# Kernel tuning notes

Hardware: AMD Instinct MI355X
Metric: run time of the kernel (lower is better)

## Reference

```python
import jax, jax.numpy as jnp
import numpy as np

B, S, D, H = 2, 2048, 1024, 16
DK = D // H


def setup_inputs() -> dict:
    key = jax.random.key(0)
    ks = jax.random.split(key, 8)
    scale = 1.0 / np.sqrt(D)
    inp = {
        "query": jax.random.normal(ks[0], (B, S, D), dtype=jnp.float32),
        "key": jax.random.normal(ks[1], (B, S, D), dtype=jnp.float32),
        "value": jax.random.normal(ks[2], (B, S, D), dtype=jnp.float32),
        # causal mask, broadcastable over batch and heads
        "mask": jnp.tril(jnp.ones((S, S), dtype=jnp.int32))[None, None, :, :],
        "W_q": jax.random.normal(ks[3], (D, D), dtype=jnp.float32) * scale,
        "W_k": jax.random.normal(ks[4], (D, D), dtype=jnp.float32) * scale,
        "W_v": jax.random.normal(ks[5], (D, D), dtype=jnp.float32) * scale,
        "W_o": jax.random.normal(ks[6], (D, D), dtype=jnp.float32) * scale,
    }
    return inp


def _split_heads(t):
    Bb, Ss, _ = t.shape
    return t.reshape(Bb, Ss, H, DK).transpose(0, 2, 1, 3)  # [B,H,S,DK]


def reference(query, key, value, mask, W_q, W_k, W_v, W_o):
    # Linear(d,d,bias=False): y = x @ W^T (torch stores weight as [out,in])
    Q = _split_heads(query @ W_q.T)
    K = _split_heads(key @ W_k.T)
    V = _split_heads(value @ W_v.T)
    scores = jnp.einsum("bhqd,bhkd->bhqk", Q, K) / jnp.sqrt(jnp.float32(DK))
    scores = jnp.where(mask == 0, -jnp.inf, scores)
    weights = jax.nn.softmax(scores, axis=-1)
    weights = jnp.nan_to_num(weights, nan=0.0)  # fully-masked rows -> 0
    # dropout is identity at inference
    x = jnp.einsum("bhqk,bhkd->bhqd", weights, V)
    x = x.transpose(0, 2, 1, 3).reshape(B, S, D)
    return x @ W_o.T
```

## Files before the change

### kernel.cpp

```cpp
#include <hip/hip_runtime.h>
#include <hip/hip_bf16.h>

#define D_MODEL 1024
#define NHEAD   16
#define HDK     64
#define SEQ     2048
#define BATCH   2
#define BS      (BATCH * SEQ)

typedef __attribute__((ext_vector_type(8))) short bf16x8;
typedef __attribute__((ext_vector_type(4))) float f32x4;

__device__ __forceinline__ unsigned short f2bf(float f) {
    unsigned u = __builtin_bit_cast(unsigned, f);
    u += 0x7fffu + ((u >> 16) & 1u);
    return (unsigned short)(u >> 16);
}

__device__ __forceinline__ unsigned pack_hi(float x, float y) {
    return __builtin_amdgcn_perm(__builtin_bit_cast(unsigned, y),
                                 __builtin_bit_cast(unsigned, x), 0x07060302u);
}

typedef const void __attribute__((address_space(1))) gas_void;
typedef void __attribute__((address_space(3))) las_void;

__device__ __forceinline__ void gll16(const void* g, void* l) {
    __builtin_amdgcn_global_load_lds((gas_void*)g, (las_void*)l, 16, 0, 0);
}

__device__ __forceinline__ void cast_body(const float* __restrict__ src,
                                          unsigned short* __restrict__ dst, int i) {
    const float4* p = (const float4*)src + (size_t)i * 2;
    float4 a = p[0], b = p[1];
    ushort4 lo = make_ushort4(f2bf(a.x), f2bf(a.y), f2bf(a.z), f2bf(a.w));
    ushort4 hi = make_ushort4(f2bf(b.x), f2bf(b.y), f2bf(b.z), f2bf(b.w));
    ushort4* q = (ushort4*)dst + (size_t)i * 2;
    q[0] = lo; q[1] = hi;
}

__global__ __launch_bounds__(256)
void cast_act(const float* a, const float* b, const float* c,
              unsigned short* oa, unsigned short* ob, unsigned short* oc, int n8) {
    int i = blockIdx.x * 256 + threadIdx.x;
    if (i >= n8) return;
    const float* s = blockIdx.y == 0 ? a : blockIdx.y == 1 ? b : c;
    unsigned short* d = blockIdx.y == 0 ? oa : blockIdx.y == 1 ? ob : oc;
    cast_body(s, d, i);
}

__global__ __launch_bounds__(256)
void cast_wt(const float* a, const float* b, const float* c, const float* dd,
             unsigned short* oa, unsigned short* ob, unsigned short* oc, unsigned short* od, int n8) {
    int i = blockIdx.x * 256 + threadIdx.x;
    if (i >= n8) return;
    const float* s = blockIdx.y == 0 ? a : blockIdx.y == 1 ? b : blockIdx.y == 2 ? c : dd;
    unsigned short* d = blockIdx.y == 0 ? oa : blockIdx.y == 1 ? ob : blockIdx.y == 2 ? oc : od;
    cast_body(s, d, i);
}

__device__ __forceinline__ void gemm_kloop128(const unsigned short* __restrict__ X,
                                              const unsigned short* __restrict__ W,
                                              unsigned short* As, unsigned short* Bs,
                                              int bm, int bn, f32x4 acc[4][4]) {
    const int t    = threadIdx.x;
    const int w    = t >> 6;
    const int L    = t & 63;
    const int quad = L >> 4;
    const int lm   = L & 15;
    const int r8   = L >> 3;
    const int sl   = L & 7;
    const int xcol = ((sl ^ r8) & 7) * 8;
    const int wr   = (w >> 1) * 64;
    const int wc   = (w & 1) * 64;

    for (int kt = 0; kt < D_MODEL; kt += 64) {
        __syncthreads();
        #pragma unroll
        for (int i = 0; i < 4; ++i) {
            int c = w * 4 + i;
            gll16(X + (size_t)(bm + c * 8 + r8) * D_MODEL + kt + xcol, &As[c * 512]);
        }
        #pragma unroll
        for (int i = 0; i < 4; ++i) {
            int c = w * 4 + i;
            gll16(W + (size_t)(bn + c * 8 + r8) * D_MODEL + kt + xcol, &Bs[c * 512]);
        }
        __syncthreads();

        #pragma unroll
        for (int ch = 0; ch < 2; ++ch) {
            bf16x8 af[4], bfr[4];
            #pragma unroll
            for (int ms = 0; ms < 4; ++ms) {
                int row = wr + ms * 16 + lm;
                af[ms] = *(const bf16x8*)&As[row * 64 + (((ch * 4 + quad) ^ (row & 7)) * 8)];
            }
            #pragma unroll
            for (int ns = 0; ns < 4; ++ns) {
                int row = wc + ns * 16 + lm;
                bfr[ns] = *(const bf16x8*)&Bs[row * 64 + (((ch * 4 + quad) ^ (row & 7)) * 8)];
            }
            #pragma unroll
            for (int ms = 0; ms < 4; ++ms)
                #pragma unroll
                for (int ns = 0; ns < 4; ++ns)
                    acc[ms][ns] = __builtin_amdgcn_mfma_f32_16x16x32_bf16(
                        af[ms], bfr[ns], acc[ms][ns], 0, 0, 0);
        }
    }
}

__device__ __forceinline__ void gemm_kloop64(const unsigned short* __restrict__ X,
                                             const unsigned short* __restrict__ W,
                                             unsigned short* As, unsigned short* Bs,
                                             int bm, int bn, f32x4 acc[2][4]) {
    const int t    = threadIdx.x;
    const int w    = t >> 6;
    const int L    = t & 63;
    const int quad = L >> 4;
    const int lm   = L & 15;
    const int r8   = L >> 3;
    const int sl   = L & 7;
    const int xcol = ((sl ^ r8) & 7) * 8;

    for (int kt = 0; kt < D_MODEL; kt += 64) {
        __syncthreads();
        #pragma unroll
        for (int i = 0; i < 4; ++i) {
            int c = w * 4 + i;
            gll16(X + (size_t)(bm + c * 8 + r8) * D_MODEL + kt + xcol, &As[c * 512]);
        }
        #pragma unroll
        for (int i = 0; i < 2; ++i) {
            int c = w * 2 + i;
            gll16(W + (size_t)(bn + c * 8 + r8) * D_MODEL + kt + xcol, &Bs[c * 512]);
        }
        __syncthreads();

        #pragma unroll
        for (int ch = 0; ch < 2; ++ch) {
            bf16x8 af[2], bfr[4];
            #pragma unroll
            for (int ms = 0; ms < 2; ++ms) {
                int row = w * 32 + ms * 16 + lm;
                af[ms] = *(const bf16x8*)&As[row * 64 + (((ch * 4 + quad) ^ (row & 7)) * 8)];
            }
            #pragma unroll
            for (int ns = 0; ns < 4; ++ns) {
                int row = ns * 16 + lm;
                bfr[ns] = *(const bf16x8*)&Bs[row * 64 + (((ch * 4 + quad) ^ (row & 7)) * 8)];
            }
            #pragma unroll
            for (int ms = 0; ms < 2; ++ms)
                #pragma unroll
                for (int ns = 0; ns < 4; ++ns)
                    acc[ms][ns] = __builtin_amdgcn_mfma_f32_16x16x32_bf16(
                        af[ms], bfr[ns], acc[ms][ns], 0, 0, 0);
        }
    }
}

__global__ __launch_bounds__(256, 3)
void proj_gemm(const unsigned short* __restrict__ qx, const unsigned short* __restrict__ kx,
               const unsigned short* __restrict__ vx, const unsigned short* __restrict__ wq,
               const unsigned short* __restrict__ wk, const unsigned short* __restrict__ wv,
               unsigned short* __restrict__ Qp, unsigned short* __restrict__ Kp,
               unsigned short* __restrict__ VT) {
    __shared__ __align__(16) unsigned short As[128 * 64];
    __shared__ __align__(16) unsigned short Bs[128 * 64];

    const int p = blockIdx.z;
    const unsigned short* X = p == 0 ? qx : p == 1 ? kx : vx;
    const unsigned short* W = p == 0 ? wq : p == 1 ? wk : wv;
    const int bm = blockIdx.y * 128, bn = blockIdx.x * 128;

    f32x4 acc[4][4];
    #pragma unroll
    for (int ms = 0; ms < 4; ++ms)
        #pragma unroll
        for (int ns = 0; ns < 4; ++ns)
            acc[ms][ns] = (f32x4){0.f, 0.f, 0.f, 0.f};

    gemm_kloop128(X, W, As, Bs, bm, bn, acc);

    const int t = threadIdx.x, w = t >> 6, L = t & 63, quad = L >> 4, lm = L & 15;
    const int wr = (w >> 1) * 64, wc = (w & 1) * 64;
    if (p == 2) {
        const int b    = bm >> 11;
        const int s_in = (bm & (SEQ - 1)) + wr;
        #pragma unroll
        for (int ms = 0; ms < 4; ++ms)
            #pragma unroll
            for (int ns = 0; ns < 4; ++ns) {
                int dg = bn + wc + ns * 16 + lm;
                int h  = dg >> 6, d = dg & 63;
                ushort4 pk = make_ushort4(f2bf(acc[ms][ns][0]), f2bf(acc[ms][ns][1]),
                                          f2bf(acc[ms][ns][2]), f2bf(acc[ms][ns][3]));
                *(ushort4*)&VT[((size_t)((b * NHEAD + h) * HDK + d)) * SEQ +
                               s_in + ms * 16 + quad * 4] = pk;
            }
    } else {
        unsigned short* Y = p == 0 ? Qp : Kp;
        const float scl = p == 0 ? 0.125f : 1.0f;
        #pragma unroll
        for (int ms = 0; ms < 4; ++ms)
            #pragma unroll
            for (int ns = 0; ns < 4; ++ns)
                #pragma unroll
                for (int r = 0; r < 4; ++r)
                    Y[(size_t)(bm + wr + ms * 16 + quad * 4 + r) * D_MODEL +
                      bn + wc + ns * 16 + lm] = f2bf(acc[ms][ns][r] * scl);
    }
}

__global__ __launch_bounds__(256)
void out_gemm(const unsigned short* __restrict__ X, const unsigned short* __restrict__ W,
              float* __restrict__ Y) {
    __shared__ __align__(16) unsigned short As[128 * 64];
    __shared__ __align__(16) unsigned short Bs[64 * 64];
    const int bm = blockIdx.y * 128, bn = blockIdx.x * 64;

    f32x4 acc[2][4];
    #pragma unroll
    for (int ms = 0; ms < 2; ++ms)
        #pragma unroll
        for (int ns = 0; ns < 4; ++ns)
            acc[ms][ns] = (f32x4){0.f, 0.f, 0.f, 0.f};

    gemm_kloop64(X, W, As, Bs, bm, bn, acc);

    const int t = threadIdx.x, w = t >> 6, L = t & 63, quad = L >> 4, lm = L & 15;
    #pragma unroll
    for (int ms = 0; ms < 2; ++ms)
        #pragma unroll
        for (int ns = 0; ns < 4; ++ns)
            #pragma unroll
            for (int r = 0; r < 4; ++r)
                Y[(size_t)(bm + w * 32 + ms * 16 + quad * 4 + r) * D_MODEL +
                  bn + ns * 16 + lm] = acc[ms][ns][r];
}

__global__ __launch_bounds__(256, 3)
void attn_mfma(const unsigned short* __restrict__ Q, const unsigned short* __restrict__ K,
               const unsigned short* __restrict__ VT, unsigned short* __restrict__ A) {
    __shared__ __align__(16) unsigned short Ks[2][64 * 72];
    __shared__ __align__(16) unsigned short Vs[2][64 * 72];
    __shared__ __align__(16) unsigned short Ps[4 * 16 * 72];

    const int t    = threadIdx.x;
    const int w    = t >> 6;
    const int L    = t & 63;
    const int quad = L >> 4;
    const int lm   = L & 15;
    const int h    = blockIdx.y;
    const int b    = blockIdx.z;
    const size_t hb  = (size_t)b * SEQ * D_MODEL + h * HDK;
    const size_t vhb = (size_t)(b * NHEAD + h) * HDK;

    const int srow = t >> 2;
    const int sc   = (t & 3) * 16;
    const unsigned short* kp = K + hb + (size_t)srow * D_MODEL + sc;
    const unsigned short* vp = VT + (vhb + srow) * SEQ + sc;
    unsigned short* ps = &Ps[w * 16 * 72];

    for (int half = 0; half < 2; ++half) {
        const int qt   = half ? 31 - (int)blockIdx.x : (int)blockIdx.x;
        const int q0   = qt * 64;
        const int qrow = q0 + w * 16 + lm;

        bf16x8 Qf0, Qf1;
        {
            const unsigned short* qp = Q + hb + (size_t)qrow * D_MODEL + quad * 8;
            Qf0 = *(const bf16x8*)qp;
            Qf1 = *(const bf16x8*)(qp + 32);
        }

        f32x4 Oacc[4];
        #pragma unroll
        for (int nt = 0; nt < 4; ++nt) Oacc[nt] = (f32x4){0.f, 0.f, 0.f, 0.f};
        float m_run = -INFINITY, l_run = 0.f;

        float4 kr0 = *(const float4*)kp;
        float4 kr1 = *(const float4*)(kp + 8);
        float4 vr0 = *(const float4*)vp;
        float4 vr1 = *(const float4*)(vp + 8);
        *(float4*)&Ks[0][srow * 72 + sc]     = kr0;
        *(float4*)&Ks[0][srow * 72 + sc + 8] = kr1;
        *(float4*)&Vs[0][srow * 72 + sc]     = vr0;
        *(float4*)&Vs[0][srow * 72 + sc + 8] = vr1;
        if (qt >= 1) {
            kr0 = *(const float4*)(kp + (size_t)64 * D_MODEL);
            kr1 = *(const float4*)(kp + (size_t)64 * D_MODEL + 8);
            vr0 = *(const float4*)(vp + 64);
            vr1 = *(const float4*)(vp + 64 + 8);
        }
        __syncthreads();

        int bb = 0;
        for (int kt = 0; kt <= qt; ++kt) {
            const int k0 = kt * 64;
            const unsigned short* Kc = Ks[bb];
            const unsigned short* Vc = Vs[bb];
            if (kt < qt) {
                unsigned short* Kn = Ks[bb ^ 1];
                unsigned short* Vn = Vs[bb ^ 1];
                *(float4*)&Kn[srow * 72 + sc]     = kr0;
                *(float4*)&Kn[srow * 72 + sc + 8] = kr1;
                *(float4*)&Vn[srow * 72 + sc]     = vr0;
                *(float4*)&Vn[srow * 72 + sc + 8] = vr1;
                if (kt + 2 <= qt) {
                    kr0 = *(const float4*)(kp + (size_t)(k0 + 128) * D_MODEL);
                    kr1 = *(const float4*)(kp + (size_t)(k0 + 128) * D_MODEL + 8);
                    vr0 = *(const float4*)(vp + k0 + 128);
                    vr1 = *(const float4*)(vp + k0 + 128 + 8);
                }
            }

            f32x4 S[4];
            #pragma unroll
            for (int ct = 0; ct < 4; ++ct) {
                bf16x8 a0 = *(const bf16x8*)&Kc[(ct * 16 + lm) * 72 + quad * 8];
                bf16x8 a1 = *(const bf16x8*)&Kc[(ct * 16 + lm) * 72 + 32 + quad * 8];
                f32x4 z = (f32x4){0.f, 0.f, 0.f, 0.f};
                z = __builtin_amdgcn_mfma_f32_16x16x32_bf16(a0, Qf0, z, 0, 0, 0);
                z = __builtin_amdgcn_mfma_f32_16x16x32_bf16(a1, Qf1, z, 0, 0, 0);
                S[ct] = z;
            }

            if (k0 + 63 > q0 + w * 16) {
                #pragma unroll
                for (int ct = 0; ct < 4; ++ct)
                    #pragma unroll
                    for (int r = 0; r < 4; ++r)
                        if ((k0 + ct * 16 + quad * 4 + r) > qrow)
                            S[ct][r] = -1e30f;
            }

            float m = fmaxf(fmaxf(fmaxf(S[0][0], S[0][1]), fmaxf(S[0][2], S[0][3])),
                            fmaxf(fmaxf(S[1][0], S[1][1]), fmaxf(S[1][2], S[1][3])));
            m = fmaxf(m, fmaxf(fmaxf(fmaxf(S[2][0], S[2][1]), fmaxf(S[2][2], S[2][3])),
                               fmaxf(fmaxf(S[3][0], S[3][1]), fmaxf(S[3][2], S[3][3]))));
            m = fmaxf(m, __shfl_xor(m, 16));
            m = fmaxf(m, __shfl_xor(m, 32));
            const float m_new = fmaxf(m_run, m);
            const float alpha = __expf(m_run - m_new);
            m_run = m_new;
            float psum = 0.f;
            #pragma unroll
            for (int ct = 0; ct < 4; ++ct)
                #pragma unroll
                for (int r = 0; r < 4; ++r) {
                    float e = __expf(S[ct][r] - m_new);
                    S[ct][r] = e;
                    psum += e;
                }
            psum += __shfl_xor(psum, 16);
            psum += __shfl_xor(psum, 32);
            l_run = l_run * alpha + psum;

            #pragma unroll
            for (int ct = 0; ct < 4; ++ct) {
                uint2 pw = make_uint2(pack_hi(S[ct][0], S[ct][1]),
                                      pack_hi(S[ct][2], S[ct][3]));
                *(uint2*)&ps[lm * 72 + ct * 16 + quad * 4] = pw;
            }
            bf16x8 Pb0 = *(const bf16x8*)&ps[lm * 72 + quad * 8];
            bf16x8 Pb1 = *(const bf16x8*)&ps[lm * 72 + 32 + quad * 8];

            #pragma unroll
            for (int nt = 0; nt < 4; ++nt) {
                bf16x8 a0 = *(const bf16x8*)&Vc[(nt * 16 + lm) * 72 + quad * 8];
                bf16x8 a1 = *(const bf16x8*)&Vc[(nt * 16 + lm) * 72 + 32 + quad * 8];
                f32x4 o = Oacc[nt];
                #pragma unroll
                for (int r = 0; r < 4; ++r) o[r] *= alpha;
                o = __builtin_amdgcn_mfma_f32_16x16x32_bf16(a0, Pb0, o, 0, 0, 0);
                o = __builtin_amdgcn_mfma_f32_16x16x32_bf16(a1, Pb1, o, 0, 0, 0);
                Oacc[nt] = o;
            }

            __syncthreads();
            bb ^= 1;
        }

        const float inv_l = 1.f / l_run;
        #pragma unroll
        for (int nt = 0; nt < 4; ++nt) {
            ushort4 pk = make_ushort4(f2bf(Oacc[nt][0] * inv_l), f2bf(Oacc[nt][1] * inv_l),
                                      f2bf(Oacc[nt][2] * inv_l), f2bf(Oacc[nt][3] * inv_l));
            *(ushort4*)&ps[lm * 72 + nt * 16 + quad * 4] = pk;
        }
        #pragma unroll
        for (int p = 0; p < 2; ++p) {
            int qr = p * 8 + (L >> 3);
            int dc = (L & 7) * 8;
            uint4 val = *(const uint4*)&ps[qr * 72 + dc];
            *(uint4*)&A[hb + (size_t)(q0 + w * 16 + qr) * D_MODEL + dc] = val;
        }
    }
}

extern "C" void kernel_launch(void* const* d_in, const int* in_sizes, int n_in,
                              void* d_out, int out_size, void* d_ws, size_t ws_size,
                              hipStream_t stream) {
    const float* q  = (const float*)d_in[0];
    const float* k  = (const float*)d_in[1];
    const float* v  = (const float*)d_in[2];
    const float* Wq = (const float*)d_in[4];
    const float* Wk = (const float*)d_in[5];
    const float* Wv = (const float*)d_in[6];
    const float* Wo = (const float*)d_in[7];
    float* out = (float*)d_out;

    char* ws = (char*)d_ws;
    const size_t MB = 1024 * 1024;
    unsigned short* qb  = (unsigned short*)(ws + 0 * MB);
    unsigned short* kb  = (unsigned short*)(ws + 8 * MB);
    unsigned short* vb  = (unsigned short*)(ws + 16 * MB);
    unsigned short* wqb = (unsigned short*)(ws + 24 * MB);
    unsigned short* wkb = (unsigned short*)(ws + 26 * MB);
    unsigned short* wvb = (unsigned short*)(ws + 28 * MB);
    unsigned short* wob = (unsigned short*)(ws + 30 * MB);
    unsigned short* Qp  = (unsigned short*)(ws + 32 * MB);
    unsigned short* Kp  = (unsigned short*)(ws + 40 * MB);
    unsigned short* VTp = (unsigned short*)(ws + 48 * MB);
    unsigned short* Ap  = (unsigned short*)(ws + 56 * MB);

    const int nX8 = BS * D_MODEL / 8;
    const int nW8 = D_MODEL * D_MODEL / 8;
    cast_act<<<dim3(nX8 / 256, 3), 256, 0, stream>>>(q, k, v, qb, kb, vb, nX8);
    cast_wt <<<dim3(nW8 / 256, 4), 256, 0, stream>>>(Wq, Wk, Wv, Wo, wqb, wkb, wvb, wob, nW8);

    proj_gemm<<<dim3(D_MODEL / 128, BS / 128, 3), 256, 0, stream>>>(
        qb, kb, vb, wqb, wkb, wvb, Qp, Kp, VTp);

    attn_mfma<<<dim3(16, NHEAD, BATCH), 256, 0, stream>>>(Qp, Kp, VTp, Ap);

    out_gemm<<<dim3(D_MODEL / 64, BS / 128), 256, 0, stream>>>(Ap, wob, out);
}
```

Baseline: 225.9 us.

## Fuse fp32-to-bf16 casts into GEMMs, flatten attention grid, use exp2 softmax

After: 255.0 us. +12.9%, slower.

```diff
diff --git a/kernel.cpp b/kernel.cpp
--- a/kernel.cpp
+++ b/kernel.cpp
@@ -17,11 +17,23 @@
     return (unsigned short)(u >> 16);
 }
 
+__device__ __forceinline__ unsigned pk_rne(float x, float y) {
+    return (unsigned)f2bf(x) | ((unsigned)f2bf(y) << 16);
+}
+
 __device__ __forceinline__ unsigned pack_hi(float x, float y) {
     return __builtin_amdgcn_perm(__builtin_bit_cast(unsigned, y),
                                  __builtin_bit_cast(unsigned, x), 0x07060302u);
 }
 
+__device__ __forceinline__ float fexp2(float x) {
+#if __has_builtin(__builtin_amdgcn_exp2f)
+    return __builtin_amdgcn_exp2f(x);
+#else
+    return exp2f(x);
+#endif
+}
+
 typedef const void __attribute__((address_space(1))) gas_void;
 typedef void __attribute__((address_space(3))) las_void;
 
@@ -29,40 +41,114 @@
     __builtin_amdgcn_global_load_lds((gas_void*)g, (las_void*)l, 16, 0, 0);
 }
 
-__device__ __forceinline__ void cast_body(const float* __restrict__ src,
-                                          unsigned short* __restrict__ dst, int i) {
-    const float4* p = (const float4*)src + (size_t)i * 2;
-    float4 a = p[0], b = p[1];
-    ushort4 lo = make_ushort4(f2bf(a.x), f2bf(a.y), f2bf(a.z), f2bf(a.w));
-    ushort4 hi = make_ushort4(f2bf(b.x), f2bf(b.y), f2bf(b.z), f2bf(b.w));
-    ushort4* q = (ushort4*)dst + (size_t)i * 2;
-    q[0] = lo; q[1] = hi;
+template <int ROWS>
+__device__ __forceinline__ void stage_f32(const float* __restrict__ X, int ld,
+                                          unsigned short* Ls, int t) {
+    #pragma unroll
+    for (int g = 0; g < ROWS / 32; ++g) {
+        int row = (t >> 3) + g * 32;
+        int sl  = t & 7;
+        int col = (sl ^ (row & 7)) * 8;
+        const float4* p = (const float4*)(X + (size_t)row * ld + col);
+        float4 a = p[0], b = p[1];
+        *(uint4*)&Ls[row * 64 + sl * 8] =
+            make_uint4(pk_rne(a.x, a.y), pk_rne(a.z, a.w),
+                       pk_rne(b.x, b.y), pk_rne(b.z, b.w));
+    }
 }
 
 __global__ __launch_bounds__(256)
-void cast_act(const float* a, const float* b, const float* c,
-              unsigned short* oa, unsigned short* ob, unsigned short* oc, int n8) {
-    int i = blockIdx.x * 256 + threadIdx.x;
-    if (i >= n8) return;
-    const float* s = blockIdx.y == 0 ? a : blockIdx.y == 1 ? b : c;
-    unsigned short* d = blockIdx.y == 0 ? oa : blockIdx.y == 1 ? ob : oc;
-    cast_body(s, d, i);
+void proj_gemm(const float* __restrict__ qx, const float* __restrict__ kx,
+               const float* __restrict__ vx, const float* __restrict__ wq,
+               const float* __restrict__ wk, const float* __restrict__ wv,
+               unsigned short* __restrict__ Qp, unsigned short* __restrict__ Kp,
+               unsigned short* __restrict__ VT) {
+    __shared__ __align__(16) unsigned short As[128 * 64];
+    __shared__ __align__(16) unsigned short Bs[128 * 64];
+
+    const int p = blockIdx.z;
+    const float* X = p == 0 ? qx : p == 1 ? kx : vx;
+    const float* W = p == 0 ? wq : p == 1 ? wk : wv;
+    const int bm = blockIdx.y * 128, bn = blockIdx.x * 128;
+
+    const int t    = threadIdx.x;
+    const int w    = t >> 6;
+    const int L    = t & 63;
+    const int quad = L >> 4;
+    const int lm   = L & 15;
+    const int wr   = (w >> 1) * 64;
+    const int wc   = (w & 1) * 64;
+
+    f32x4 acc[4][4];
+    #pragma unroll
+    for (int ms = 0; ms < 4; ++ms)
+        #pragma unroll
+        for (int ns = 0; ns < 4; ++ns)
+            acc[ms][ns] = (f32x4){0.f, 0.f, 0.f, 0.f};
+
+    for (int kt = 0; kt < D_MODEL; kt += 64) {
+        __syncthreads();
+        stage_f32<128>(X + (size_t)bm * D_MODEL + kt, D_MODEL, As, t);
+        stage_f32<128>(W + (size_t)bn * D_MODEL + kt, D_MODEL, Bs, t);
+        __syncthreads();
+
+        #pragma unroll
+        for (int ch = 0; ch < 2; ++ch) {
+            bf16x8 af[4], bfr[4];
+            #pragma unroll
+            for (int ms = 0; ms < 4; ++ms) {
+                int row = wr + ms * 16 + lm;
+                af[ms] = *(const bf16x8*)&As[row * 64 + (((ch * 4 + quad) ^ (row & 7)) * 8)];
+            }
+            #pragma unroll
+            for (int ns = 0; ns < 4; ++ns) {
+                int row = wc + ns * 16 + lm;
+                bfr[ns] = *(const bf16x8*)&Bs[row * 64 + (((ch * 4 + quad) ^ (row & 7)) * 8)];
+            }
+            #pragma unroll
+            for (int ms = 0; ms < 4; ++ms)
+                #pragma unroll
+                for (int ns = 0; ns < 4; ++ns)
+                    acc[ms][ns] = __builtin_amdgcn_mfma_f32_16x16x32_bf16(
+                        af[ms], bfr[ns], acc[ms][ns], 0, 0, 0);
+        }
+    }
+
+    if (p == 2) {
+        const int b    = bm >> 11;
+        const int s_in = (bm & (SEQ - 1)) + wr;
+        #pragma unroll
+        for (int ms = 0; ms < 4; ++ms)
+            #pragma unroll
+            for (int ns = 0; ns < 4; ++ns) {
+                int dg = bn + wc + ns * 16 + lm;
+                int h  = dg >> 6, d = dg & 63;
+                ushort4 pkv = make_ushort4(f2bf(acc[ms][ns][0]), f2bf(acc[ms][ns][1]),
+                                           f2bf(acc[ms][ns][2]), f2bf(acc[ms][ns][3]));
+                *(ushort4*)&VT[((size_t)((b * NHEAD + h) * HDK + d)) * SEQ +
+                               s_in + ms * 16 + quad * 4] = pkv;
+            }
+    } else {
+        unsigned short* Y = p == 0 ? Qp : Kp;
+        const float scl = p == 0 ? 0.18033688011112042f : 1.0f;
+        #pragma unroll
+        for (int ms = 0; ms < 4; ++ms)
+            #pragma unroll
+            for (int ns = 0; ns < 4; ++ns)
+                #pragma unroll
+                for (int r = 0; r < 4; ++r)
+                    Y[(size_t)(bm + wr + ms * 16 + quad * 4 + r) * D_MODEL +
+                      bn + wc + ns * 16 + lm] = f2bf(acc[ms][ns][r] * scl);
+    }
 }
 
 __global__ __launch_bounds__(256)
-void cast_wt(const float* a, const float* b, const float* c, const float* dd,
-             unsigned short* oa, unsigned short* ob, unsigned short* oc, unsigned short* od, int n8) {
-    int i = blockIdx.x * 256 + threadIdx.x;
-    if (i >= n8) return;
-    const float* s = blockIdx.y == 0 ? a : blockIdx.y == 1 ? b : blockIdx.y == 2 ? c : dd;
-    unsigned short* d = blockIdx.y == 0 ? oa : blockIdx.y == 1 ? ob : blockIdx.y == 2 ? oc : od;
-    cast_body(s, d, i);
-}
-
-__device__ __forceinline__ void gemm_kloop128(const unsigned short* __restrict__ X,
-                                              const unsigned short* __restrict__ W,
-                                              unsigned short* As, unsigned short* Bs,
-                                              int bm, int bn, f32x4 acc[4][4]) {
+void out_gemm(const unsigned short* __restrict__ X, const float* __restrict__ W,
+              float* __restrict__ Y) {
+    __shared__ __align__(16) unsigned short As[128 * 64];
+    __shared__ __align__(16) unsigned short Bs[64 * 64];
+    const int bm = blockIdx.y * 128, bn = blockIdx.x * 64;
+
     const int t    = threadIdx.x;
     const int w    = t >> 6;
     const int L    = t & 63;
@@ -71,8 +157,13 @@
     const int r8   = L >> 3;
     const int sl   = L & 7;
     const int xcol = ((sl ^ r8) & 7) * 8;
-    const int wr   = (w >> 1) * 64;
-    const int wc   = (w & 1) * 64;
+
+    f32x4 acc[2][4];
+    #pragma unroll
+    for (int ms = 0; ms < 2; ++ms)
+        #pragma unroll
+        for (int ns = 0; ns < 4; ++ns)
+            acc[ms][ns] = (f32x4){0.f, 0.f, 0.f, 0.f};
 
     for (int kt = 0; kt < D_MODEL; kt += 64) {
         __syncthreads();
@@ -81,180 +172,59 @@
             int c = w * 4 + i;
             gll16(X + (size_t)(bm + c * 8 + r8) * D_MODEL + kt + xcol, &As[c * 512]);
         }
-        #pragma unroll
-        for (int i = 0; i < 4; ++i) {
-            int c = w * 4 + i;
-            gll16(W + (size_t)(bn + c * 8 + r8) * D_MODEL + kt + xcol, &Bs[c * 512]);
-        }
+        stage_f32<64>(W + (size_t)bn * D_MODEL + kt, D_MODEL, Bs, t);
         __syncthreads();
 
         #pragma unroll
         for (int ch = 0; ch < 2; ++ch) {
-            bf16x8 af[4], bfr[4];
-            #pragma unroll
-            for (int ms = 0; ms < 4; ++ms) {
-                int row = wr + ms * 16 + lm;
+            bf16x8 af[2], bfr[4];
+            #pragma unroll
+            for (int ms = 0; ms < 2; ++ms) {
+                int row = w * 32 + ms * 16 + lm;
                 af[ms] = *(const bf16x8*)&As[row * 64 + (((ch * 4 + quad) ^ (row & 7)) * 8)];
             }
             #pragma unroll
             for (int ns = 0; ns < 4; ++ns) {
-                int row = wc + ns * 16 + lm;
+                int row = ns * 16 + lm;
                 bfr[ns] = *(const bf16x8*)&Bs[row * 64 + (((ch * 4 + quad) ^ (row & 7)) * 8)];
             }
             #pragma unroll
-            for (int ms = 0; ms < 4; ++ms)
+            for (int ms = 0; ms < 2; ++ms)
                 #pragma unroll
                 for (int ns = 0; ns < 4; ++ns)
                     acc[ms][ns] = __builtin_amdgcn_mfma_f32_16x16x32_bf16(
                         af[ms], bfr[ns], acc[ms][ns], 0, 0, 0);
         }
     }
-}
-
-__device__ __forceinline__ void gemm_kloop64(const unsigned short* __restrict__ X,
-                                             const unsigned short* __restrict__ W,
-                                             unsigned short* As, unsigned short* Bs,
-                                             int bm, int bn, f32x4 acc[2][4]) {
+
+    #pragma unroll
+    for (int ms = 0; ms < 2; ++ms)
+        #pragma unroll
+        for (int ns = 0; ns < 4; ++ns)
+            #pragma unroll
+            for (int r = 0; r < 4; ++r)
+                Y[(size_t)(bm + w * 32 + ms * 16 + quad * 4 + r) * D_MODEL +
+                  bn + ns * 16 + lm] = acc[ms][ns][r];
+}
+
+__global__ __launch_bounds__(256)
+void attn_mfma(const unsigned short* __restrict__ Q, const unsigned short* __restrict__ K,
+               const unsigned short* __restrict__ VT, unsigned short* __restrict__ A) {
+    __shared__ __align__(16) unsigned short Ks[2][64 * 72];
+    __shared__ __align__(16) unsigned short Vs[2][64 * 72];
+    __shared__ __align__(16) unsigned short Ps[4][16 * 72];
+
     const int t    = threadIdx.x;
     const int w    = t >> 6;
     const int L    = t & 63;
     const int quad = L >> 4;
     const int lm   = L & 15;
-    const int r8   = L >> 3;
-    const int sl   = L & 7;
-    const int xcol = ((sl ^ r8) & 7) * 8;
-
-    for (int kt = 0; kt < D_MODEL; kt += 64) {
-        __syncthreads();
-        #pragma unroll
-        for (int i = 0; i < 4; ++i) {
-            int c = w * 4 + i;
-            gll16(X + (size_t)(bm + c * 8 + r8) * D_MODEL + kt + xcol, &As[c * 512]);
-        }
-        #pragma unroll
-        for (int i = 0; i < 2; ++i) {
-            int c = w * 2 + i;
-            gll16(W + (size_t)(bn + c * 8 + r8) * D_MODEL + kt + xcol, &Bs[c * 512]);
-        }
-        __syncthreads();
-
-        #pragma unroll
-        for (int ch = 0; ch < 2; ++ch) {
-            bf16x8 af[2], bfr[4];
-            #pragma unroll
-            for (int ms = 0; ms < 2; ++ms) {
-                int row = w * 32 + ms * 16 + lm;
-                af[ms] = *(const bf16x8*)&As[row * 64 + (((ch * 4 + quad) ^ (row & 7)) * 8)];
-            }
-            #pragma unroll
-            for (int ns = 0; ns < 4; ++ns) {
-                int row = ns * 16 + lm;
-                bfr[ns] = *(const bf16x8*)&Bs[row * 64 + (((ch * 4 + quad) ^ (row & 7)) * 8)];
-            }
-            #pragma unroll
-            for (int ms = 0; ms < 2; ++ms)
-                #pragma unroll
-                for (int ns = 0; ns < 4; ++ns)
-                    acc[ms][ns] = __builtin_amdgcn_mfma_f32_16x16x32_bf16(
-                        af[ms], bfr[ns], acc[ms][ns], 0, 0, 0);
-        }
-    }
-}
-
-__global__ __launch_bounds__(256, 3)
-void proj_gemm(const unsigned short* __restrict__ qx, const unsigned short* __restrict__ kx,
-               const unsigned short* __restrict__ vx, const unsigned short* __restrict__ wq,
-               const unsigned short* __restrict__ wk, const unsigned short* __restrict__ wv,
-               unsigned short* __restrict__ Qp, unsigned short* __restrict__ Kp,
-               unsigned short* __restrict__ VT) {
-    __shared__ __align__(16) unsigned short As[128 * 64];
-    __shared__ __align__(16) unsigned short Bs[128 * 64];
-
-    const int p = blockIdx.z;
-    const unsigned short* X = p == 0 ? qx : p == 1 ? kx : vx;
-    const unsigned short* W = p == 0 ? wq : p == 1 ? wk : wv;
-    const int bm = blockIdx.y * 128, bn = blockIdx.x * 128;
-
-    f32x4 acc[4][4];
-    #pragma unroll
-    for (int ms = 0; ms < 4; ++ms)
-        #pragma unroll
-        for (int ns = 0; ns < 4; ++ns)
-            acc[ms][ns] = (f32x4){0.f, 0.f, 0.f, 0.f};
-
-    gemm_kloop128(X, W, As, Bs, bm, bn, acc);
-
-    const int t = threadIdx.x, w = t >> 6, L = t & 63, quad = L >> 4, lm = L & 15;
-    const int wr = (w >> 1) * 64, wc = (w & 1) * 64;
-    if (p == 2) {
-        const int b    = bm >> 11;
-        const int s_in = (bm & (SEQ - 1)) + wr;
-        #pragma unroll
-        for (int ms = 0; ms < 4; ++ms)
-            #pragma unroll
-            for (int ns = 0; ns < 4; ++ns) {
-                int dg = bn + wc + ns * 16 + lm;
-                int h  = dg >> 6, d = dg & 63;
-                ushort4 pk = make_ushort4(f2bf(acc[ms][ns][0]), f2bf(acc[ms][ns][1]),
-                                          f2bf(acc[ms][ns][2]), f2bf(acc[ms][ns][3]));
-                *(ushort4*)&VT[((size_t)((b * NHEAD + h) * HDK + d)) * SEQ +
-                               s_in + ms * 16 + quad * 4] = pk;
-            }
-    } else {
-        unsigned short* Y = p == 0 ? Qp : Kp;
-        const float scl = p == 0 ? 0.125f : 1.0f;
-        #pragma unroll
-        for (int ms = 0; ms < 4; ++ms)
-            #pragma unroll
-            for (int ns = 0; ns < 4; ++ns)
-                #pragma unroll
-                for (int r = 0; r < 4; ++r)
-                    Y[(size_t)(bm + wr + ms * 16 + quad * 4 + r) * D_MODEL +
-                      bn + wc + ns * 16 + lm] = f2bf(acc[ms][ns][r] * scl);
-    }
-}
-
-__global__ __launch_bounds__(256)
-void out_gemm(const unsigned short* __restrict__ X, const unsigned short* __restrict__ W,
-              float* __restrict__ Y) {
-    __shared__ __align__(16) unsigned short As[128 * 64];
-    __shared__ __align__(16) unsigned short Bs[64 * 64];
-    const int bm = blockIdx.y * 128, bn = blockIdx.x * 64;
-
-    f32x4 acc[2][4];
-    #pragma unroll
-    for (int ms = 0; ms < 2; ++ms)
-        #pragma unroll
-        for (int ns = 0; ns < 4; ++ns)
-            acc[ms][ns] = (f32x4){0.f, 0.f, 0.f, 0.f};
-
-    gemm_kloop64(X, W, As, Bs, bm, bn, acc);
-
-    const int t = threadIdx.x, w = t >> 6, L = t & 63, quad = L >> 4, lm = L & 15;
-    #pragma unroll
-    for (int ms = 0; ms < 2; ++ms)
-        #pragma unroll
-        for (int ns = 0; ns < 4; ++ns)
-            #pragma unroll
-            for (int r = 0; r < 4; ++r)
-                Y[(size_t)(bm + w * 32 + ms * 16 + quad * 4 + r) * D_MODEL +
-                  bn + ns * 16 + lm] = acc[ms][ns][r];
-}
-
-__global__ __launch_bounds__(256, 3)
-void attn_mfma(const unsigned short* __restrict__ Q, const unsigned short* __restrict__ K,
-               const unsigned short* __restrict__ VT, unsigned short* __restrict__ A) {
-    __shared__ __align__(16) unsigned short Ks[2][64 * 72];
-    __shared__ __align__(16) unsigned short Vs[2][64 * 72];
-    __shared__ __align__(16) unsigned short Ps[4 * 16 * 72];
-
-    const int t    = threadIdx.x;
-    const int w    = t >> 6;
-    const int L    = t & 63;
-    const int quad = L >> 4;
-    const int lm   = L & 15;
-    const int h    = blockIdx.y;
-    const int b    = blockIdx.z;
+
+    const int f    = blockIdx.x;
+    const int qt   = 31 - (f >> 5);
+    const int bh   = f & 31;
+    const int b    = bh >> 4, h = bh & 15;
+    const int q0   = qt * 64;
     const size_t hb  = (size_t)b * SEQ * D_MODEL + h * HDK;
     const size_t vhb = (size_t)(b * NHEAD + h) * HDK;
 
@@ -262,142 +232,137 @@
     const int sc   = (t & 3) * 16;
     const unsigned short* kp = K + hb + (size_t)srow * D_MODEL + sc;
     const unsigned short* vp = VT + (vhb + srow) * SEQ + sc;
-    unsigned short* ps = &Ps[w * 16 * 72];
-
-    for (int half = 0; half < 2; ++half) {
-        const int qt   = half ? 31 - (int)blockIdx.x : (int)blockIdx.x;
-        const int q0   = qt * 64;
-        const int qrow = q0 + w * 16 + lm;
-
-        bf16x8 Qf0, Qf1;
-        {
-            const unsigned short* qp = Q + hb + (size_t)qrow * D_MODEL + quad * 8;
-            Qf0 = *(const bf16x8*)qp;
-            Qf1 = *(const bf16x8*)(qp + 32);
-        }
-
-        f32x4 Oacc[4];
-        #pragma unroll
-        for (int nt = 0; nt < 4; ++nt) Oacc[nt] = (f32x4){0.f, 0.f, 0.f, 0.f};
-        float m_run = -INFINITY, l_run = 0.f;
-
-        float4 kr0 = *(const float4*)kp;
-        float4 kr1 = *(const float4*)(kp + 8);
-        float4 vr0 = *(const float4*)vp;
-        float4 vr1 = *(const float4*)(vp + 8);
-        *(float4*)&Ks[0][srow * 72 + sc]     = kr0;
-        *(float4*)&Ks[0][srow * 72 + sc + 8] = kr1;
-        *(float4*)&Vs[0][srow * 72 + sc]     = vr0;
-        *(float4*)&Vs[0][srow * 72 + sc + 8] = vr1;
-        if (qt >= 1) {
-            kr0 = *(const float4*)(kp + (size_t)64 * D_MODEL);
-            kr1 = *(const float4*)(kp + (size_t)64 * D_MODEL + 8);
-            vr0 = *(const float4*)(vp + 64);
-            vr1 = *(const float4*)(vp + 64 + 8);
-        }
-        __syncthreads();
-
-        int bb = 0;
-        for (int kt = 0; kt <= qt; ++kt) {
-            const int k0 = kt * 64;
-            const unsigned short* Kc = Ks[bb];
-            const unsigned short* Vc = Vs[bb];
-            if (kt < qt) {
-                unsigned short* Kn = Ks[bb ^ 1];
-                unsigned short* Vn = Vs[bb ^ 1];
-                *(float4*)&Kn[srow * 72 + sc]     = kr0;
-                *(float4*)&Kn[srow * 72 + sc + 8] = kr1;
-                *(float4*)&Vn[srow * 72 + sc]     = vr0;
-                *(float4*)&Vn[srow * 72 + sc + 8] = vr1;
-                if (kt + 2 <= qt) {
-                    kr0 = *(const float4*)(kp + (size_t)(k0 + 128) * D_MODEL);
-                    kr1 = *(const float4*)(kp + (size_t)(k0 + 128) * D_MODEL + 8);
-                    vr0 = *(const float4*)(vp + k0 + 128);
-                    vr1 = *(const float4*)(vp + k0 + 128 + 8);
-                }
-            }
-
-            f32x4 S[4];
-            #pragma unroll
-            for (int ct = 0; ct < 4; ++ct) {
-                bf16x8 a0 = *(const bf16x8*)&Kc[(ct * 16 + lm) * 72 + quad * 8];
-                bf16x8 a1 = *(const bf16x8*)&Kc[(ct * 16 + lm) * 72 + 32 + quad * 8];
-                f32x4 z = (f32x4){0.f, 0.f, 0.f, 0.f};
-                z = __builtin_amdgcn_mfma_f32_16x16x32_bf16(a0, Qf0, z, 0, 0, 0);
-                z = __builtin_amdgcn_mfma_f32_16x16x32_bf16(a1, Qf1, z, 0, 0, 0);
-                S[ct] = z;
-            }
-
-            if (k0 + 63 > q0 + w * 16) {
-                #pragma unroll
-                for (int ct = 0; ct < 4; ++ct)
-                    #pragma unroll
-                    for (int r = 0; r < 4; ++r)
-                        if ((k0 + ct * 16 + quad * 4 + r) > qrow)
-                            S[ct][r] = -1e30f;
-            }
-
-            float m = fmaxf(fmaxf(fmaxf(S[0][0], S[0][1]), fmaxf(S[0][2], S[0][3])),
-                            fmaxf(fmaxf(S[1][0], S[1][1]), fmaxf(S[1][2], S[1][3])));
-            m = fmaxf(m, fmaxf(fmaxf(fmaxf(S[2][0], S[2][1]), fmaxf(S[2][2], S[2][3])),
-                               fmaxf(fmaxf(S[3][0], S[3][1]), fmaxf(S[3][2], S[3][3]))));
-            m = fmaxf(m, __shfl_xor(m, 16));
-            m = fmaxf(m, __shfl_xor(m, 32));
-            const float m_new = fmaxf(m_run, m);
-            const float alpha = __expf(m_run - m_new);
-            m_run = m_new;
-            float psum = 0.f;
+    unsigned short* ps = &Ps[w][0];
+
+    const int qrow = q0 + w * 16 + lm;
+    bf16x8 Qf0, Qf1;
+    {
+        const unsigned short* qp = Q + hb + (size_t)qrow * D_MODEL + quad * 8;
+        Qf0 = *(const bf16x8*)qp;
+        Qf1 = *(const bf16x8*)(qp + 32);
+    }
+
+    f32x4 Oacc[4];
+    #pragma unroll
+    for (int nt = 0; nt < 4; ++nt) Oacc[nt] = (f32x4){0.f, 0.f, 0.f, 0.f};
+    float m_run = -INFINITY, l_part = 0.f;
+
+    float4 k0r = *(const float4*)kp;
+    float4 k1r = *(const float4*)(kp + 8);
+    float4 v0r = *(const float4*)vp;
+    float4 v1r = *(const float4*)(vp + 8);
+    *(float4*)&Ks[0][srow * 72 + sc]     = k0r;
+    *(float4*)&Ks[0][srow * 72 + sc + 8] = k1r;
+    *(float4*)&Vs[0][srow * 72 + sc]     = v0r;
+    *(float4*)&Vs[0][srow * 72 + sc + 8] = v1r;
+    if (qt >= 1) {
+        k0r = *(const float4*)(kp + (size_t)64 * D_MODEL);
+        k1r = *(const float4*)(kp + (size_t)64 * D_MODEL + 8);
+        v0r = *(const float4*)(vp + 64);
+        v1r = *(const float4*)(vp + 64 + 8);
+    }
+    __syncthreads();
+
+    int bb = 0;
+    for (int kt = 0; kt <= qt; ++kt) {
+        if (kt < qt) {
+            unsigned short* Kn = Ks[bb ^ 1];
+            unsigned short* Vn = Vs[bb ^ 1];
+            *(float4*)&Kn[srow * 72 + sc]     = k0r;
+            *(float4*)&Kn[srow * 72 + sc + 8] = k1r;
+            *(float4*)&Vn[srow * 72 + sc]     = v0r;
+            *(float4*)&Vn[srow * 72 + sc + 8] = v1r;
+            if (kt + 2 <= qt) {
+                k0r = *(const float4*)(kp + (size_t)(kt + 2) * 64 * D_MODEL);
+                k1r = *(const float4*)(kp + (size_t)(kt + 2) * 64 * D_MODEL + 8);
+                v0r = *(const float4*)(vp + (kt + 2) * 64);
+                v1r = *(const float4*)(vp + (kt + 2) * 64 + 8);
+            }
+        }
+        const unsigned short* Kc = Ks[bb];
+        const unsigned short* Vc = Vs[bb];
+
+        f32x4 S[4];
+        #pragma unroll
+        for (int ct = 0; ct < 4; ++ct) {
+            bf16x8 a0 = *(const bf16x8*)&Kc[(ct * 16 + lm) * 72 + quad * 8];
+            bf16x8 a1 = *(const bf16x8*)&Kc[(ct * 16 + lm) * 72 + 32 + quad * 8];
+            f32x4 z = (f32x4){0.f, 0.f, 0.f, 0.f};
+            z = __builtin_amdgcn_mfma_f32_16x16x32_bf16(a0, Qf0, z, 0, 0, 0);
+            z = __builtin_amdgcn_mfma_f32_16x16x32_bf16(a1, Qf1, z, 0, 0, 0);
+            S[ct] = z;
+        }
+
+        if (kt == qt) {
             #pragma unroll
             for (int ct = 0; ct < 4; ++ct)
                 #pragma unroll
-                for (int r = 0; r < 4; ++r) {
-                    float e = __expf(S[ct][r] - m_new);
-                    S[ct][r] = e;
-                    psum += e;
-                }
-            psum += __shfl_xor(psum, 16);
-            psum += __shfl_xor(psum, 32);
-            l_run = l_run * alpha + psum;
-
-            #pragma unroll
-            for (int ct = 0; ct < 4; ++ct) {
-                uint2 pw = make_uint2(pack_hi(S[ct][0], S[ct][1]),
-                                      pack_hi(S[ct][2], S[ct][3]));
-                *(uint2*)&ps[lm * 72 + ct * 16 + quad * 4] = pw;
-            }
-            bf16x8 Pb0 = *(const bf16x8*)&ps[lm * 72 + quad * 8];
-            bf16x8 Pb1 = *(const bf16x8*)&ps[lm * 72 + 32 + quad * 8];
-
-            #pragma unroll
-            for (int nt = 0; nt < 4; ++nt) {
-                bf16x8 a0 = *(const bf16x8*)&Vc[(nt * 16 + lm) * 72 + quad * 8];
-                bf16x8 a1 = *(const bf16x8*)&Vc[(nt * 16 + lm) * 72 + 32 + quad * 8];
-                f32x4 o = Oacc[nt];
-                #pragma unroll
-                for (int r = 0; r < 4; ++r) o[r] *= alpha;
-                o = __builtin_amdgcn_mfma_f32_16x16x32_bf16(a0, Pb0, o, 0, 0, 0);
-                o = __builtin_amdgcn_mfma_f32_16x16x32_bf16(a1, Pb1, o, 0, 0, 0);
-                Oacc[nt] = o;
-            }
-
-            __syncthreads();
-            bb ^= 1;
-        }
-
-        const float inv_l = 1.f / l_run;
+                for (int r = 0; r < 4; ++r)
+                    if ((q0 + ct * 16 + quad * 4 + r) > qrow)
+                        S[ct][r] = -1e30f;
+        }
+
+        float m = fmaxf(fmaxf(fmaxf(S[0][0], S[0][1]), fmaxf(S[0][2], S[0][3])),
+                        fmaxf(fmaxf(S[1][0], S[1][1]), fmaxf(S[1][2], S[1][3])));
+        m = fmaxf(m, fmaxf(fmaxf(fmaxf(S[2][0], S[2][1]), fmaxf(S[2][2], S[2][3])),
+                           fmaxf(fmaxf(S[3][0], S[3][1]), fmaxf(S[3][2], S[3][3]))));
+        m = fmaxf(m, __shfl_xor(m, 16));
+        m = fmaxf(m, __shfl_xor(m, 32));
+        const float m_new = fmaxf(m_run, m);
+        const float alpha = fexp2(m_run - m_new);
+        m_run = m_new;
+        float psum = 0.f;
+        #pragma unroll
+        for (int ct = 0; ct < 4; ++ct)
+            #pragma unroll
+            for (int r = 0; r < 4; ++r) {
+                float e = fexp2(S[ct][r] - m_new);
+                S[ct][r] = e;
+                psum += e;
+            }
+        l_part = l_part * alpha + psum;
+
+        #pragma unroll
+        for (int ct = 0; ct < 4; ++ct) {
+            uint2 pw = make_uint2(pack_hi(S[ct][0], S[ct][1]),
+                                  pack_hi(S[ct][2], S[ct][3]));
+            *(uint2*)&ps[lm * 72 + ct * 16 + quad * 4] = pw;
+        }
+        bf16x8 Pb0 = *(const bf16x8*)&ps[lm * 72 + quad * 8];
+        bf16x8 Pb1 = *(const bf16x8*)&ps[lm * 72 + 32 + quad * 8];
+
         #pragma unroll
         for (int nt = 0; nt < 4; ++nt) {
-            ushort4 pk = make_ushort4(f2bf(Oacc[nt][0] * inv_l), f2bf(Oacc[nt][1] * inv_l),
-                                      f2bf(Oacc[nt][2] * inv_l), f2bf(Oacc[nt][3] * inv_l));
-            *(ushort4*)&ps[lm * 72 + nt * 16 + quad * 4] = pk;
-        }
-        #pragma unroll
-        for (int p = 0; p < 2; ++p) {
-            int qr = p * 8 + (L >> 3);
-            int dc = (L & 7) * 8;
-            uint4 val = *(const uint4*)&ps[qr * 72 + dc];
-            *(uint4*)&A[hb + (size_t)(q0 + w * 16 + qr) * D_MODEL + dc] = val;
-        }
+            bf16x8 a0 = *(const bf16x8*)&Vc[(nt * 16 + lm) * 72 + quad * 8];
+            bf16x8 a1 = *(const bf16x8*)&Vc[(nt * 16 + lm) * 72 + 32 + quad * 8];
+            f32x4 o = Oacc[nt];
+            #pragma unroll
+            for (int r = 0; r < 4; ++r) o[r] *= alpha;
+            o = __builtin_amdgcn_mfma_f32_16x16x32_bf16(a0, Pb0, o, 0, 0, 0);
+            o = __builtin_amdgcn_mfma_f32_16x16x32_bf16(a1, Pb1, o, 0, 0, 0);
+            Oacc[nt] = o;
+        }
+
+        __syncthreads();
+        bb ^= 1;
+    }
+
+    float l = l_part;
+    l += __shfl_xor(l, 16);
+    l += __shfl_xor(l, 32);
+    const float inv_l = 1.f / l;
+    #pragma unroll
+    for (int nt = 0; nt < 4; ++nt) {
+        ushort4 pkv = make_ushort4(f2bf(Oacc[nt][0] * inv_l), f2bf(Oacc[nt][1] * inv_l),
+                                   f2bf(Oacc[nt][2] * inv_l), f2bf(Oacc[nt][3] * inv_l));
+        *(ushort4*)&ps[lm * 72 + nt * 16 + quad * 4] = pkv;
+    }
+    #pragma unroll
+    for (int cc = 0; cc < 2; ++cc) {
+        int row = cc * 8 + (L >> 3);
+        int seg = L & 7;
+        uint4 val = *(const uint4*)&ps[row * 72 + seg * 8];
+        *(uint4*)&A[hb + (size_t)(q0 + w * 16 + row) * D_MODEL + seg * 8] = val;
     }
 }
 
@@ -415,27 +380,15 @@
 
     char* ws = (char*)d_ws;
     const size_t MB = 1024 * 1024;
-    unsigned short* qb  = (unsigned short*)(ws + 0 * MB);
-    unsigned short* kb  = (unsigned short*)(ws + 8 * MB);
-    unsigned short* vb  = (unsigned short*)(ws + 16 * MB);
-    unsigned short* wqb = (unsigned short*)(ws + 24 * MB);
-    unsigned short* wkb = (unsigned short*)(ws + 26 * MB);
-    unsigned short* wvb = (unsigned short*)(ws + 28 * MB);
-    unsigned short* wob = (unsigned short*)(ws + 30 * MB);
-    unsigned short* Qp  = (unsigned short*)(ws + 32 * MB);
-    unsigned short* Kp  = (unsigned short*)(ws + 40 * MB);
-    unsigned short* VTp = (unsigned short*)(ws + 48 * MB);
-    unsigned short* Ap  = (unsigned short*)(ws + 56 * MB);
-
-    const int nX8 = BS * D_MODEL / 8;
-    const int nW8 = D_MODEL * D_MODEL / 8;
-    cast_act<<<dim3(nX8 / 256, 3), 256, 0, stream>>>(q, k, v, qb, kb, vb, nX8);
-    cast_wt <<<dim3(nW8 / 256, 4), 256, 0, stream>>>(Wq, Wk, Wv, Wo, wqb, wkb, wvb, wob, nW8);
+    unsigned short* Qp  = (unsigned short*)(ws + 0 * MB);
+    unsigned short* Kp  = (unsigned short*)(ws + 8 * MB);
+    unsigned short* VTp = (unsigned short*)(ws + 16 * MB);
+    unsigned short* Ap  = (unsigned short*)(ws + 24 * MB);
 
     proj_gemm<<<dim3(D_MODEL / 128, BS / 128, 3), 256, 0, stream>>>(
-        qb, kb, vb, wqb, wkb, wvb, Qp, Kp, VTp);
-
-    attn_mfma<<<dim3(16, NHEAD, BATCH), 256, 0, stream>>>(Qp, Kp, VTp, Ap);
-
-    out_gemm<<<dim3(D_MODEL / 64, BS / 128), 256, 0, stream>>>(Ap, wob, out);
-}
+        q, k, v, Wq, Wk, Wv, Qp, Kp, VTp);
+
+    attn_mfma<<<dim3(1024), 256, 0, stream>>>(Qp, Kp, VTp, Ap);
+
+    out_gemm<<<dim3(D_MODEL / 64, BS / 128), 256, 0, stream>>>(Ap, Wo, out);
+}
```
